# Kernel tuning notes

Hardware: AMD Instinct MI355X
Metric: run time of the kernel (lower is better)

Reference implementation:

```python
import jax, jax.numpy as jnp
import numpy as np

N_NODES = 50000
N_RAND_EDGES = 800000
D = 128


def setup_inputs() -> dict:
    key = jax.random.key(0)
    ks = jax.random.split(key, 16)
    # random edges + self loops (docstring: self loops added to avoid zero in-degree)
    src_r = jax.random.randint(ks[0], (N_RAND_EDGES,), 0, N_NODES, dtype=jnp.int32)
    dst_r = jax.random.randint(ks[1], (N_RAND_EDGES,), 0, N_NODES, dtype=jnp.int32)
    loop = jnp.arange(N_NODES, dtype=jnp.int32)
    src = jnp.concatenate([src_r, loop])
    dst = jnp.concatenate([dst_r, loop])
    E = src.shape[0]
    edge_weight = jax.random.uniform(ks[2], (E,), dtype=jnp.float32, minval=0.05, maxval=1.0)
    feats = jax.random.normal(ks[3], (N_NODES, D), dtype=jnp.float32)
    s = 1.0 / np.sqrt(D)
    params = {}
    for i in range(3):
        params[f'W_self{i}'] = jax.random.normal(ks[4 + 3 * i], (D, D), dtype=jnp.float32) * s
        params[f'W_neigh{i}'] = jax.random.normal(ks[5 + 3 * i], (D, D), dtype=jnp.float32) * s
        params[f'b{i}'] = jnp.zeros((D,), dtype=jnp.float32)
    return dict(feats=feats, edge_weight=edge_weight,
                W_self0=params['W_self0'], W_neigh0=params['W_neigh0'], b0=params['b0'],
                W_self1=params['W_self1'], W_neigh1=params['W_neigh1'], b1=params['b1'],
                W_self2=params['W_self2'], W_neigh2=params['W_neigh2'], b2=params['b2'],
                src=src, dst=dst)


def reference(feats, edge_weight, W_self0, W_neigh0, b0, W_self1, W_neigh1, b1,
              W_self2, W_neigh2, b2, src, dst):
    N = feats.shape[0]
    seg = lambda x, ids: jax.ops.segment_sum(x, ids, num_segments=N)
    # EdgeWeightNorm('both'): w_ij / sqrt(out_deg_w(src) * in_deg_w(dst))
    deg_dst = seg(edge_weight, dst)  # weighted in-degree [N]
    deg_src = seg(edge_weight, src)  # weighted out-degree [N]
    denom = jnp.sqrt(jnp.maximum(deg_src[src] * deg_dst[dst], 1e-12))
    w = edge_weight / denom  # [E]
    # unweighted in-degree for DGL fn.mean
    in_deg = jnp.maximum(seg(jnp.ones_like(edge_weight), dst), 1.0)  # [N]

    def sage_layer(h, Ws, Wn, b, act):
        # GraphNorm(None) is identity. SAGEConv mean aggregator with edge weights:
        # m_e = w_e * h[src_e]; neigh_v = mean over in-edges of v
        msgs = w[:, None] * h[src]            # [E, D] (memory-bound gather)
        neigh = seg(msgs, dst) / in_deg[:, None]  # [N, D]
        out = h @ Ws + neigh @ Wn + b
        return jax.nn.relu(out) if act else out

    h = sage_layer(feats, W_self0, W_neigh0, b0, True)
    h = sage_layer(h, W_self1, W_neigh1, b1, True)
    h = sage_layer(h, W_self2, W_neigh2, b2, False)
    return h
```

## Files before the change

### kernel.cpp

```cpp
#include <hip/hip_runtime.h>
#include <hip/hip_bf16.h>

#define D 128
#define BS 256
#define CHUNK 4096
#define CAP 8192

typedef __attribute__((ext_vector_type(8))) short short8v;
typedef __attribute__((ext_vector_type(4))) float f32x4;

__device__ __forceinline__ ushort f2bf(float f) {
    uint u = __float_as_uint(f);
    return (ushort)((u + 0x7fffu + ((u >> 16) & 1u)) >> 16);
}
__device__ __forceinline__ float bf2f(ushort s) {
    return __uint_as_float(((uint)s) << 16);
}


__global__ void cvt_all(const float* __restrict__ feats,
                        const float* __restrict__ Ws0, const float* __restrict__ Wn0,
                        const float* __restrict__ Ws1, const float* __restrict__ Wn1,
                        const float* __restrict__ Ws2, const float* __restrict__ Wn2,
                        ushort* __restrict__ hb, ushort* __restrict__ Wt,
                        int* __restrict__ cursD, int* __restrict__ cursS,
                        int n8, int FB) {
    int tid = threadIdx.x;
    if (blockIdx.x == 0) {
        cursD[tid] = tid * CAP;
        cursS[tid] = tid * CAP;
    }
    if (blockIdx.x < FB) {
        int i = blockIdx.x * 256 + tid;
        if (i >= n8) return;
        const float4* f4 = (const float4*)feats + (size_t)i * 2;
        float4 a = f4[0], b = f4[1];
        uint4 o;
        o.x = (uint)f2bf(a.x) | ((uint)f2bf(a.y) << 16);
        o.y = (uint)f2bf(a.z) | ((uint)f2bf(a.w) << 16);
        o.z = (uint)f2bf(b.x) | ((uint)f2bf(b.y) << 16);
        o.w = (uint)f2bf(b.z) | ((uint)f2bf(b.w) << 16);
        *((uint4*)hb + i) = o;
        return;
    }
    int wb = blockIdx.x - FB;
    int layer = wb >> 7;
    int n = wb & 127;
    int k = tid;
    const float* Ws = (layer == 0) ? Ws0 : (layer == 1) ? Ws1 : Ws2;
    const float* Wn = (layer == 0) ? Wn0 : (layer == 1) ? Wn1 : Wn2;
    float v = (k < 128) ? Ws[k * D + n] : Wn[(k - 128) * D + n];
    Wt[(size_t)layer * 32768 + n * 256 + k] = f2bf(v);
}


__global__ void partition_kernel(const int* __restrict__ src, const int* __restrict__ dst,
                                 const float* __restrict__ ew,
                                 int* __restrict__ cursD, int* __restrict__ cursS,
                                 int2* __restrict__ bufD, int2* __restrict__ bufS, int E) {
    __shared__ int hD[256], hS[256];
    __shared__ int bD[256], bS[256];
    int tid = threadIdx.x, blk = blockIdx.x;
    hD[tid] = 0; hS[tid] = 0;
    __syncthreads();
    int e0 = blk * CHUNK;
    int e1 = e0 + CHUNK < E ? e0 + CHUNK : E;
    for (int e = e0 + tid; e < e1; e += BS) {
        atomicAdd(&hD[dst[e] >> 8], 1);
        atomicAdd(&hS[src[e] >> 8], 1);
    }
    __syncthreads();
    int cD = hD[tid], cS = hS[tid];
    if (cD > 0) bD[tid] = atomicAdd(&cursD[tid], cD);
    if (cS > 0) bS[tid] = atomicAdd(&cursS[tid], cS);
    __syncthreads();
    for (int e = e0 + tid; e < e1; e += BS) {
        int s = src[e], d = dst[e];
        int w = __float_as_int(ew[e]);
        int pD = atomicAdd(&bD[d >> 8], 1);
        bufD[pD] = make_int2(((d & 255) << 16) | s, w);
        int pS = atomicAdd(&bS[s >> 8], 1);
        bufS[pS] = make_int2(s, w);
    }
}


__global__ void srcdeg_kernel(const int2* __restrict__ bufS, const int* __restrict__ cursS,
                              float* __restrict__ rs, int N) {
    __shared__ float acc[256];
    int tid = threadIdx.x, b = blockIdx.x;
    acc[tid] = 0.f;
    __syncthreads();
    int base = b * CAP;
    int end = cursS[b];
    for (int i = base + tid; i < end; i += BS) {
        int2 v = bufS[i];
        atomicAdd(&acc[v.x & 255], __int_as_float(v.y));
    }
    __syncthreads();
    int node = (b << 8) + tid;
    if (node < N) rs[node] = rsqrtf(acc[tid]);
}


__global__ void csr_kernel(const int2* __restrict__ bufD, const int* __restrict__ cursD,
                           const float* __restrict__ rs, int2* __restrict__ begend,
                           int2* __restrict__ csrb, int N) {
    __shared__ int lcnt[256];
    __shared__ float lw[256];
    __shared__ int sc[256];
    int tid = threadIdx.x, b = blockIdx.x;
    lcnt[tid] = 0; lw[tid] = 0.f;
    __syncthreads();
    int base = b * CAP;
    int end = cursD[b];
    for (int i = base + tid; i < end; i += BS) {
        int2 v = bufD[i];
        int l = v.x >> 16;
        atomicAdd(&lcnt[l], 1);
        atomicAdd(&lw[l], __int_as_float(v.y));
    }
    __syncthreads();
    int myc = lcnt[tid];
    float myw = lw[tid];
    sc[tid] = myc;
    __syncthreads();
    for (int off = 1; off < 256; off <<= 1) {
        int t = (tid >= off) ? sc[tid - off] : 0;
        __syncthreads();
        sc[tid] += t;
        __syncthreads();
    }
    int lbase = base + sc[tid] - myc;
    int node = (b << 8) + tid;
    if (node < N) begend[node] = make_int2(lbase, base + sc[tid]);
    lcnt[tid] = lbase;
    lw[tid] = (myc > 0) ? rsqrtf(myw) / (float)myc : 0.f;
    __syncthreads();
    for (int i = base + tid; i < end; i += BS) {
        int2 v = bufD[i];
        int l = v.x >> 16;
        int s = v.x & 0xFFFF;
        float w = __int_as_float(v.y) * rs[s] * lw[l];
        int p = atomicAdd(&lcnt[l], 1);
        csrb[p] = make_int2(s, __float_as_int(w));
    }
}


__global__ void aggregate_bf(const ushort* __restrict__ h, const int2* __restrict__ begend,
                             const int2* __restrict__ csr, ushort* __restrict__ nb, int N) {
    int node = (blockIdx.x * blockDim.x + threadIdx.x) >> 6;
    int lane = threadIdx.x & 63;
    if (node >= N) return;
    int2 be = begend[node];
    int beg = be.x, end = be.y;
    float ax0 = 0.f, ay0 = 0.f, ax1 = 0.f, ay1 = 0.f;
    float ax2 = 0.f, ay2 = 0.f, ax3 = 0.f, ay3 = 0.f;
    int i = beg;
    for (; i + 4 <= end; i += 4) {
        int2 e0 = csr[i], e1 = csr[i + 1], e2 = csr[i + 2], e3 = csr[i + 3];
        float w0 = __int_as_float(e0.y), w1 = __int_as_float(e1.y);
        float w2 = __int_as_float(e2.y), w3 = __int_as_float(e3.y);
        uint x0 = *(const uint*)(h + (size_t)e0.x * D + 2 * lane);
        uint x1 = *(const uint*)(h + (size_t)e1.x * D + 2 * lane);
        uint x2 = *(const uint*)(h + (size_t)e2.x * D + 2 * lane);
        uint x3 = *(const uint*)(h + (size_t)e3.x * D + 2 * lane);
        ax0 += w0 * bf2f((ushort)x0); ay0 += w0 * bf2f((ushort)(x0 >> 16));
        ax1 += w1 * bf2f((ushort)x1); ay1 += w1 * bf2f((ushort)(x1 >> 16));
        ax2 += w2 * bf2f((ushort)x2); ay2 += w2 * bf2f((ushort)(x2 >> 16));
        ax3 += w3 * bf2f((ushort)x3); ay3 += w3 * bf2f((ushort)(x3 >> 16));
    }
    for (; i < end; ++i) {
        int2 e0 = csr[i];
        float w0 = __int_as_float(e0.y);
        uint x0 = *(const uint*)(h + (size_t)e0.x * D + 2 * lane);
        ax0 += w0 * bf2f((ushort)x0); ay0 += w0 * bf2f((ushort)(x0 >> 16));
    }
    float rx = (ax0 + ax1) + (ax2 + ax3);
    float ry = (ay0 + ay1) + (ay2 + ay3);
    uint o = (uint)f2bf(rx) | ((uint)f2bf(ry) << 16);
    *(uint*)(nb + (size_t)node * D + 2 * lane) = o;
}


#define AST2 40

__global__ __launch_bounds__(256) void mfma_gemm(
    const ushort* __restrict__ A1, const ushort* __restrict__ A2,
    const ushort* __restrict__ Wt, const float* __restrict__ bias,
    ushort* __restrict__ outb, float* __restrict__ outf, int N, int relu) {
    __shared__ ushort As[2][128][AST2];
    __shared__ ushort Bs[2][128][AST2];

    int tid = threadIdx.x;
    int lane = tid & 63;
    int w = tid >> 6;
    int m0 = (w >> 1) * 64, n0 = (w & 1) * 64;
    int row0 = blockIdx.x * 128;
    int q = lane >> 4, li = lane & 15;

    int r1 = tid >> 2, c = tid & 3;
    int gr1 = min(row0 + r1, N - 1);
    int gr2 = min(row0 + r1 + 64, N - 1);

    uint4 sa0, sa1, sb0, sb1;

    sa0 = *(const uint4*)(A1 + (size_t)gr1 * D + c * 8);
    sa1 = *(const uint4*)(A1 + (size_t)gr2 * D + c * 8);
    sb0 = *(const uint4*)(Wt + (size_t)r1 * 256 + c * 8);
    sb1 = *(const uint4*)(Wt + (size_t)(r1 + 64) * 256 + c * 8);
    *(uint4*)&As[0][r1][c * 8] = sa0;
    *(uint4*)&As[0][r1 + 64][c * 8] = sa1;
    *(uint4*)&Bs[0][r1][c * 8] = sb0;
    *(uint4*)&Bs[0][r1 + 64][c * 8] = sb1;
    __syncthreads();

    f32x4 zero = {0.f, 0.f, 0.f, 0.f};
    f32x4 acc[4][4];
    #pragma unroll
    for (int mf = 0; mf < 4; ++mf)
        #pragma unroll
        for (int nf = 0; nf < 4; ++nf) acc[mf][nf] = zero;

    for (int kc = 0; kc < 8; ++kc) {
        int b = kc & 1;
        if (kc < 7) {
            int nc = kc + 1;
            const ushort* Ak = ((nc < 4) ? A1 : A2) + (nc & 3) * 32;
            sa0 = *(const uint4*)(Ak + (size_t)gr1 * D + c * 8);
            sa1 = *(const uint4*)(Ak + (size_t)gr2 * D + c * 8);
            const ushort* Wk = Wt + nc * 32;
            sb0 = *(const uint4*)(Wk + (size_t)r1 * 256 + c * 8);
            sb1 = *(const uint4*)(Wk + (size_t)(r1 + 64) * 256 + c * 8);
        }

        union FragU { uint2 u[2]; short8v v; };
        FragU fa[4], fb[4];
        #pragma unroll
        for (int mf = 0; mf < 4; ++mf) {
            const ushort* p = &As[b][m0 + mf * 16 + li][0];
            fa[mf].u[0] = *(const uint2*)(p + 4 * q);
            fa[mf].u[1] = *(const uint2*)(p + 16 + 4 * q);
        }
        #pragma unroll
        for (int nf = 0; nf < 4; ++nf) {
            const ushort* p = &Bs[b][n0 + nf * 16 + li][0];
            fb[nf].u[0] = *(const uint2*)(p + 4 * q);
            fb[nf].u[1] = *(const uint2*)(p + 16 + 4 * q);
        }
        #pragma unroll
        for (int mf = 0; mf < 4; ++mf)
            #pragma unroll
            for (int nf = 0; nf < 4; ++nf)
                acc[mf][nf] = __builtin_amdgcn_mfma_f32_16x16x32_bf16(
                    fa[mf].v, fb[nf].v, acc[mf][nf], 0, 0, 0);

        if (kc < 7) {
            int b2 = b ^ 1;
            *(uint4*)&As[b2][r1][c * 8] = sa0;
            *(uint4*)&As[b2][r1 + 64][c * 8] = sa1;
            *(uint4*)&Bs[b2][r1][c * 8] = sb0;
            *(uint4*)&Bs[b2][r1 + 64][c * 8] = sb1;
        }
        __syncthreads();
    }

    #pragma unroll
    for (int nf = 0; nf < 4; ++nf) {
        int n = n0 + nf * 16 + li;
        float bn = bias[n];
        #pragma unroll
        for (int mf = 0; mf < 4; ++mf) {
            #pragma unroll
            for (int p = 0; p < 4; ++p) {
                int gr = row0 + m0 + mf * 16 + q * 4 + p;
                if (gr >= N) continue;
                float v = acc[mf][nf][p] + bn;
                if (relu) v = fmaxf(v, 0.f);
                if (outf) outf[(size_t)gr * D + n] = v;
                else outb[(size_t)gr * D + n] = f2bf(v);
            }
        }
    }
}


extern "C" void kernel_launch(void* const* d_in, const int* in_sizes, int n_in,
                              void* d_out, int out_size, void* d_ws, size_t ws_size,
                              hipStream_t stream) {
    const float* feats = (const float*)d_in[0];
    const float* ew    = (const float*)d_in[1];
    const float* Wself[3]  = {(const float*)d_in[2], (const float*)d_in[5], (const float*)d_in[8]};
    const float* Wneigh[3] = {(const float*)d_in[3], (const float*)d_in[6], (const float*)d_in[9]};
    const float* bias[3]   = {(const float*)d_in[4], (const float*)d_in[7], (const float*)d_in[10]};
    const int* src = (const int*)d_in[11];
    const int* dst = (const int*)d_in[12];

    int N = in_sizes[0] / D;
    int E = in_sizes[11];
    int NB = (N + 255) >> 8;
    int EB = (E + CHUNK - 1) / CHUNK;

    char* ws = (char*)d_ws;
    size_t p = 0;
    auto align256 = [&]() { p = (p + 255) & ~(size_t)255; };

    int* cursD = (int*)(ws + p); p += 256 * 4;             align256();
    int* cursS = (int*)(ws + p); p += 256 * 4;             align256();
    int2* bufD = (int2*)(ws + p); p += (size_t)NB * CAP * 8; align256();
    int2* bufS = (int2*)(ws + p); p += (size_t)NB * CAP * 8; align256();
    int2* csrb = (int2*)(ws + p); p += (size_t)NB * CAP * 8; align256();
    int2* begend = (int2*)(ws + p); p += (size_t)N * 8;    align256();
    float* rs  = (float*)(ws + p); p += (size_t)N * 4;     align256();
    ushort* hA = (ushort*)(ws + p); p += (size_t)N * D * 2; align256();
    ushort* hB = (ushort*)(ws + p); p += (size_t)N * D * 2; align256();
    ushort* nb = (ushort*)(ws + p); p += (size_t)N * D * 2; align256();
    ushort* Wt = (ushort*)(ws + p); p += (size_t)3 * 128 * 256 * 2; align256();
    (void)ws_size; (void)n_in; (void)out_size;

    int n8 = N * D / 8;
    int FB = (n8 + 255) / 256;
    cvt_all<<<FB + 384, 256, 0, stream>>>(feats, Wself[0], Wneigh[0], Wself[1], Wneigh[1],
                                          Wself[2], Wneigh[2], hA, Wt, cursD, cursS, n8, FB);
    partition_kernel<<<EB, BS, 0, stream>>>(src, dst, ew, cursD, cursS, bufD, bufS, E);
    srcdeg_kernel<<<NB, BS, 0, stream>>>(bufS, cursS, rs, N);
    csr_kernel<<<NB, BS, 0, stream>>>(bufD, cursD, rs, begend, csrb, N);

    int gb = (N + 127) / 128;
    ushort* hin = hA;
    ushort* houts[3] = {hB, hA, nullptr};
    for (int Lr = 0; Lr < 3; ++Lr) {
        aggregate_bf<<<(N + 3) / 4, 256, 0, stream>>>(hin, begend, csrb, nb, N);
        mfma_gemm<<<gb, 256, 0, stream>>>(hin, nb, Wt + (size_t)Lr * 32768, bias[Lr],
                                          houts[Lr], (Lr == 2) ? (float*)d_out : nullptr,
                                          N, (Lr < 2) ? 1 : 0);
        hin = houts[Lr];
    }
}
```

Baseline: 231.9 us.

## Store features column-blocked and aggregate in four 32-column passes

Hidden features and neighbor aggregates are stored column-blocked: four slabs of N×32 bf16, one per 32-column block. The aggregation kernel now runs four passes, one per slab. In each pass, four lane groups of 16 handle different edges, so each gathered row is a 64-byte segment, and the partial sums are combined with shuffles. Each pass touches a slab a quarter the size of the full feature matrix, which is meant to improve cache hit rates on the random gathers. The cost is reading the CSR four times per layer and doing more launches' worth of block work. The GEMM and conversion kernels are adjusted to read and write the new layout.

```diff
diff --git a/kernel.cpp b/kernel.cpp
--- a/kernel.cpp
+++ b/kernel.cpp
@@ -16,6 +16,7 @@
 __device__ __forceinline__ float bf2f(ushort s) {
     return __uint_as_float(((uint)s) << 16);
 }
+
 
 
 __global__ void cvt_all(const float* __restrict__ feats,
@@ -24,7 +25,7 @@
                         const float* __restrict__ Ws2, const float* __restrict__ Wn2,
                         ushort* __restrict__ hb, ushort* __restrict__ Wt,
                         int* __restrict__ cursD, int* __restrict__ cursS,
-                        int n8, int FB) {
+                        int N, int n8, int FB) {
     int tid = threadIdx.x;
     if (blockIdx.x == 0) {
         cursD[tid] = tid * CAP;
@@ -40,7 +41,9 @@
         o.y = (uint)f2bf(a.z) | ((uint)f2bf(a.w) << 16);
         o.z = (uint)f2bf(b.x) | ((uint)f2bf(b.y) << 16);
         o.w = (uint)f2bf(b.z) | ((uint)f2bf(b.w) << 16);
-        *((uint4*)hb + i) = o;
+        int node = i >> 4, c8 = i & 15;
+        ushort* op = hb + ((size_t)(c8 >> 2) * N + node) * 32 + (c8 & 3) * 8;
+        *(uint4*)op = o;
         return;
     }
     int wb = blockIdx.x - FB;
@@ -149,38 +152,44 @@
 
 
 __global__ void aggregate_bf(const ushort* __restrict__ h, const int2* __restrict__ begend,
-                             const int2* __restrict__ csr, ushort* __restrict__ nb, int N) {
-    int node = (blockIdx.x * blockDim.x + threadIdx.x) >> 6;
+                             const int2* __restrict__ csr, ushort* __restrict__ nbuf,
+                             int N, int NBLK) {
+    int pass = blockIdx.x / NBLK;
+    int nb0 = blockIdx.x - pass * NBLK;
+    int node = nb0 * 4 + (threadIdx.x >> 6);
     int lane = threadIdx.x & 63;
+    int g = lane >> 4, c = lane & 15;
     if (node >= N) return;
     int2 be = begend[node];
-    int beg = be.x, end = be.y;
-    float ax0 = 0.f, ay0 = 0.f, ax1 = 0.f, ay1 = 0.f;
-    float ax2 = 0.f, ay2 = 0.f, ax3 = 0.f, ay3 = 0.f;
-    int i = beg;
-    for (; i + 4 <= end; i += 4) {
-        int2 e0 = csr[i], e1 = csr[i + 1], e2 = csr[i + 2], e3 = csr[i + 3];
-        float w0 = __int_as_float(e0.y), w1 = __int_as_float(e1.y);
-        float w2 = __int_as_float(e2.y), w3 = __int_as_float(e3.y);
-        uint x0 = *(const uint*)(h + (size_t)e0.x * D + 2 * lane);
-        uint x1 = *(const uint*)(h + (size_t)e1.x * D + 2 * lane);
-        uint x2 = *(const uint*)(h + (size_t)e2.x * D + 2 * lane);
-        uint x3 = *(const uint*)(h + (size_t)e3.x * D + 2 * lane);
-        ax0 += w0 * bf2f((ushort)x0); ay0 += w0 * bf2f((ushort)(x0 >> 16));
-        ax1 += w1 * bf2f((ushort)x1); ay1 += w1 * bf2f((ushort)(x1 >> 16));
-        ax2 += w2 * bf2f((ushort)x2); ay2 += w2 * bf2f((ushort)(x2 >> 16));
-        ax3 += w3 * bf2f((ushort)x3); ay3 += w3 * bf2f((ushort)(x3 >> 16));
-    }
-    for (; i < end; ++i) {
-        int2 e0 = csr[i];
-        float w0 = __int_as_float(e0.y);
-        uint x0 = *(const uint*)(h + (size_t)e0.x * D + 2 * lane);
-        ax0 += w0 * bf2f((ushort)x0); ay0 += w0 * bf2f((ushort)(x0 >> 16));
-    }
-    float rx = (ax0 + ax1) + (ax2 + ax3);
-    float ry = (ay0 + ay1) + (ay2 + ay3);
-    uint o = (uint)f2bf(rx) | ((uint)f2bf(ry) << 16);
-    *(uint*)(nb + (size_t)node * D + 2 * lane) = o;
+    const uint* hs = (const uint*)h + (size_t)pass * N * 16;
+    float ax = 0.f, ay = 0.f, bx = 0.f, by = 0.f;
+    int i = be.x + g;
+    for (; i + 4 < be.y; i += 8) {
+        long long e0 = __builtin_nontemporal_load((const long long*)(csr + i));
+        long long e1 = __builtin_nontemporal_load((const long long*)(csr + i + 4));
+        int s0 = (int)(e0 & 0xFFFFFFFFll);
+        int s1 = (int)(e1 & 0xFFFFFFFFll);
+        float w0 = __int_as_float((int)(e0 >> 32));
+        float w1 = __int_as_float((int)(e1 >> 32));
+        uint x0 = hs[(size_t)s0 * 16 + c];
+        uint x1 = hs[(size_t)s1 * 16 + c];
+        ax += w0 * bf2f((ushort)x0); ay += w0 * bf2f((ushort)(x0 >> 16));
+        bx += w1 * bf2f((ushort)x1); by += w1 * bf2f((ushort)(x1 >> 16));
+    }
+    for (; i < be.y; i += 4) {
+        long long e0 = __builtin_nontemporal_load((const long long*)(csr + i));
+        int s0 = (int)(e0 & 0xFFFFFFFFll);
+        float w0 = __int_as_float((int)(e0 >> 32));
+        uint x0 = hs[(size_t)s0 * 16 + c];
+        ax += w0 * bf2f((ushort)x0); ay += w0 * bf2f((ushort)(x0 >> 16));
+    }
+    float sx = ax + bx, sy = ay + by;
+    sx += __shfl_xor(sx, 16); sy += __shfl_xor(sy, 16);
+    sx += __shfl_xor(sx, 32); sy += __shfl_xor(sy, 32);
+    if (g == 0) {
+        uint o = (uint)f2bf(sx) | ((uint)f2bf(sy) << 16);
+        ((uint*)nbuf)[(size_t)pass * N * 16 + (size_t)node * 16 + c] = o;
+    }
 }
 
 
@@ -206,8 +215,8 @@
 
     uint4 sa0, sa1, sb0, sb1;
 
-    sa0 = *(const uint4*)(A1 + (size_t)gr1 * D + c * 8);
-    sa1 = *(const uint4*)(A1 + (size_t)gr2 * D + c * 8);
+    sa0 = *(const uint4*)(A1 + (size_t)gr1 * 32 + c * 8);
+    sa1 = *(const uint4*)(A1 + (size_t)gr2 * 32 + c * 8);
     sb0 = *(const uint4*)(Wt + (size_t)r1 * 256 + c * 8);
     sb1 = *(const uint4*)(Wt + (size_t)(r1 + 64) * 256 + c * 8);
     *(uint4*)&As[0][r1][c * 8] = sa0;
@@ -227,9 +236,10 @@
         int b = kc & 1;
         if (kc < 7) {
             int nc = kc + 1;
-            const ushort* Ak = ((nc < 4) ? A1 : A2) + (nc & 3) * 32;
-            sa0 = *(const uint4*)(Ak + (size_t)gr1 * D + c * 8);
-            sa1 = *(const uint4*)(Ak + (size_t)gr2 * D + c * 8);
+            const ushort* Ak = (nc < 4) ? (A1 + (size_t)nc * N * 32)
+                                        : (A2 + (size_t)(nc - 4) * N * 32);
+            sa0 = *(const uint4*)(Ak + (size_t)gr1 * 32 + c * 8);
+            sa1 = *(const uint4*)(Ak + (size_t)gr2 * 32 + c * 8);
             const ushort* Wk = Wt + nc * 32;
             sb0 = *(const uint4*)(Wk + (size_t)r1 * 256 + c * 8);
             sb1 = *(const uint4*)(Wk + (size_t)(r1 + 64) * 256 + c * 8);
@@ -279,7 +289,7 @@
                 float v = acc[mf][nf][p] + bn;
                 if (relu) v = fmaxf(v, 0.f);
                 if (outf) outf[(size_t)gr * D + n] = v;
-                else outb[(size_t)gr * D + n] = f2bf(v);
+                else outb[((size_t)(n >> 5) * N + gr) * 32 + (n & 31)] = f2bf(v);
             }
         }
     }
@@ -315,24 +325,25 @@
     float* rs  = (float*)(ws + p); p += (size_t)N * 4;     align256();
     ushort* hA = (ushort*)(ws + p); p += (size_t)N * D * 2; align256();
     ushort* hB = (ushort*)(ws + p); p += (size_t)N * D * 2; align256();
-    ushort* nb = (ushort*)(ws + p); p += (size_t)N * D * 2; align256();
+    ushort* nbuf = (ushort*)(ws + p); p += (size_t)N * D * 2; align256();
     ushort* Wt = (ushort*)(ws + p); p += (size_t)3 * 128 * 256 * 2; align256();
     (void)ws_size; (void)n_in; (void)out_size;
 
     int n8 = N * D / 8;
     int FB = (n8 + 255) / 256;
     cvt_all<<<FB + 384, 256, 0, stream>>>(feats, Wself[0], Wneigh[0], Wself[1], Wneigh[1],
-                                          Wself[2], Wneigh[2], hA, Wt, cursD, cursS, n8, FB);
+                                          Wself[2], Wneigh[2], hA, Wt, cursD, cursS, N, n8, FB);
     partition_kernel<<<EB, BS, 0, stream>>>(src, dst, ew, cursD, cursS, bufD, bufS, E);
     srcdeg_kernel<<<NB, BS, 0, stream>>>(bufS, cursS, rs, N);
     csr_kernel<<<NB, BS, 0, stream>>>(bufD, cursD, rs, begend, csrb, N);
 
     int gb = (N + 127) / 128;
+    int NBLK = (N + 3) / 4;
     ushort* hin = hA;
     ushort* houts[3] = {hB, hA, nullptr};
     for (int Lr = 0; Lr < 3; ++Lr) {
-        aggregate_bf<<<(N + 3) / 4, 256, 0, stream>>>(hin, begend, csrb, nb, N);
-        mfma_gemm<<<gb, 256, 0, stream>>>(hin, nb, Wt + (size_t)Lr * 32768, bias[Lr],
+        aggregate_bf<<<4 * NBLK, 256, 0, stream>>>(hin, begend, csrb, nbuf, N, NBLK);
+        mfma_gemm<<<gb, 256, 0, stream>>>(hin, nbuf, Wt + (size_t)Lr * 32768, bias[Lr],
                                           houts[Lr], (Lr == 2) ? (float*)d_out : nullptr,
                                           N, (Lr < 2) ? 1 : 0);
         hin = houts[Lr];
```

Measured after the change: 407.0 us. 1.76x slower.
